# Kernel tuning notes

Measured on AMD Instinct MI355X. Metric: run time of the kernel, lower is better.

The kernel has to match this reference:

```python
import jax, jax.numpy as jnp
import numpy as np

ROI = 116
FEAT = ROI * (ROI - 1) // 2  # 6670 upper-triangular entries
D = 1024
H = 1024
EPS = 1e-5


def _batchnorm(x, gamma, beta):
    # training-mode BatchNorm1d: biased batch statistics over dim 0
    mu = jnp.mean(x, axis=0, keepdims=True)
    var = jnp.var(x, axis=0, keepdims=True)
    return (x - mu) * jax.lax.rsqrt(var + EPS) * gamma + beta


def setup_inputs() -> dict:
    key = jax.random.key(0)
    ks = jax.random.split(key, 16)
    B, W = 64, 128
    s_feat = 1.0 / np.sqrt(FEAT)
    s_d = 1.0 / np.sqrt(D)
    s_cat = 1.0 / np.sqrt(FEAT + H)
    s_h = 1.0 / np.sqrt(H)
    return {
        "FC": jax.random.normal(ks[0], (B, W, ROI, ROI), jnp.float32),
        "cluster_centers": jax.random.normal(ks[1], (2, FEAT), jnp.float32),
        # MIL attention MLP: Linear(6670,1024) -> Tanh -> Linear(1024,1)
        "W1": jax.random.uniform(ks[2], (FEAT, D), jnp.float32, -s_feat, s_feat),
        "b1": jnp.zeros((D,), jnp.float32),
        "W2": jax.random.uniform(ks[3], (D, 1), jnp.float32, -s_d, s_d),
        "b2": jnp.zeros((1,), jnp.float32),
        # batch norms
        "bn_g": jnp.ones((FEAT,), jnp.float32),
        "bn_b": jnp.zeros((FEAT,), jnp.float32),
        "bn2_g": jnp.ones((FEAT,), jnp.float32),
        "bn2_b": jnp.zeros((FEAT,), jnp.float32),
        # cross-attention projections (Wv_cross is dead code in the source)
        "Wq": jax.random.uniform(ks[4], (FEAT, H), jnp.float32, -s_feat, s_feat),
        "bq": jnp.zeros((H,), jnp.float32),
        "Wk": jax.random.uniform(ks[5], (FEAT, H), jnp.float32, -s_feat, s_feat),
        "bk": jnp.zeros((H,), jnp.float32),
        # classifier (dropout = identity at inference)
        "Wc1": jax.random.uniform(ks[6], (FEAT + H, H), jnp.float32, -s_cat, s_cat),
        "bc1": jnp.zeros((H,), jnp.float32),
        "Wc2": jax.random.uniform(ks[7], (H, 1), jnp.float32, -s_h, s_h),
        "bc2": jnp.zeros((1,), jnp.float32),
    }


def reference(FC, cluster_centers, W1, b1, W2, b2, bn_g, bn_b, bn2_g, bn2_b,
              Wq, bq, Wk, bk, Wc1, bc1, Wc2, bc2):
    iu0, iu1 = jnp.triu_indices(ROI, k=1)
    bag_level = FC[:, :, iu0, iu1]                      # [B, W, 6670]

    # MIL attention pooling, batched over samples (replaces per-sample loop)
    h = jnp.tanh(jnp.einsum('bwf,fd->bwd', bag_level, W1) + b1)
    a = jnp.einsum('bwd,dk->bwk', h, W2) + b2           # [B, W, 1]
    att = jax.nn.softmax(a[..., 0], axis=-1)            # softmax over windows
    bag_z_up = jnp.einsum('bw,bwf->bf', att, bag_level)  # [B, 6670]

    bag_z_up = _batchnorm(bag_z_up, bn_g, bn_b)
    cc = _batchnorm(cluster_centers, bn2_g, bn2_b)       # [K, 6670]

    q = bag_z_up @ Wq + bq                               # [B, H]
    k = cc @ Wk + bk                                     # [K, H]
    QK = (q @ k.T) / jnp.sqrt(jnp.float32(H))            # [B, K]
    att_cross = jax.nn.softmax(QK, axis=-1)
    v = cc @ Wq + bq                                     # NB: source reuses Wq_cross
    final_cross = att_cross @ v                          # [B, H]

    X = jnp.concatenate([final_cross, bag_z_up], axis=1)  # [B, H+6670]
    Y_prob = jax.nn.sigmoid(jax.nn.relu(X @ Wc1 + bc1) @ Wc2 + bc2)[:, 0]
    Y_hat = (Y_prob >= 0.5).astype(jnp.float32)
    return Y_prob, Y_hat
```

## Files before the change

kernel.cpp:

```cpp
#include <hip/hip_runtime.h>
#include <hip/hip_bf16.h>
#include <math.h>
#include <stdint.h>

#define ROI   116
#define FEATN 6670
#define KP    6688
#define DD    1024
#define HHN   1024
#define BB    64
#define WW    128
#define MT    8192
#define XW    7694
#define EPSV  1e-5f
#define KB_SPLIT 32

typedef __attribute__((ext_vector_type(8))) short short8;
typedef __attribute__((ext_vector_type(4))) short short4v;
typedef __attribute__((ext_vector_type(4))) float f32x4;
typedef __attribute__((ext_vector_type(4))) unsigned int u32x4;

typedef __attribute__((address_space(3))) unsigned int as3_u32;
typedef __attribute__((address_space(1))) unsigned int as1_u32;

__device__ __forceinline__ void gload_lds16(const void* g, void* l) {
  __builtin_amdgcn_global_load_lds(
      (const as1_u32*)(uintptr_t)g,
      (as3_u32*)(unsigned int)(uintptr_t)l,
      16, 0, 0);
}

__device__ __forceinline__ short f2bf(float v) {
  __hip_bfloat16 b = __float2bfloat16(v);
  return *reinterpret_cast<short*>(&b);
}

__device__ __forceinline__ float bf2f(short h) {
  unsigned int u = ((unsigned int)(unsigned short)h) << 16;
  float f;
  __builtin_memcpy(&f, &u, 4);
  return f;
}

__device__ __forceinline__ float fast_tanh(float x) {
  float ax = fabsf(x);
  float t  = __expf(-2.0f * ax);
  float r  = (1.0f - t) / (1.0f + t);
  return copysignf(r, x);
}

__global__ void k_lut(int2* lut) {
  int f = blockIdx.x * 256 + threadIdx.x;
  if (f >= FEATN) return;
  int i = (int)((231.0 - sqrt((double)(53361 - 8 * f))) * 0.5);
  if (i < 0) i = 0;
  if (i > ROI - 2) i = ROI - 2;
  while (i > 0 && i * (231 - i) / 2 > f) --i;
  while (i < ROI - 2 && (i + 1) * (231 - (i + 1)) / 2 <= f) ++i;
  int j = i + 1 + (f - i * (231 - i) / 2);
  lut[f] = make_int2(i, j);
}

__global__ void k_extract(const float* __restrict__ FC, const int2* __restrict__ lut,
                          short* __restrict__ bag, float* __restrict__ a_out) {
  int m = blockIdx.x;
  if (threadIdx.x == 0) a_out[m] = 0.f;
  const float* base = FC + (size_t)m * (ROI * ROI);
  for (int f0 = threadIdx.x * 4; f0 < KP; f0 += 1024) {
    short4v o;
#pragma unroll
    for (int e = 0; e < 4; e++) {
      int f = f0 + e;
      float v = 0.f;
      if (f < FEATN) {
        int2 ij = lut[f];
        v = base[ij.x * ROI + ij.y];
      }
      o[e] = f2bf(v);
    }
    *(short4v*)(&bag[(size_t)m * KP + f0]) = o;
  }
}

__global__ void k_transpose(const float* __restrict__ W1, short* __restrict__ W1T) {
  __shared__ float tile[32][33];
  int k0 = blockIdx.x * 32;
  int d0 = blockIdx.y * 32;
  int tx = threadIdx.x & 31, ty = threadIdx.x >> 5;
  for (int r = 0; r < 32; r += 8) {
    int k = k0 + ty + r;
    float v = 0.f;
    if (k < FEATN) v = W1[(size_t)k * DD + d0 + tx];
    tile[ty + r][tx] = v;
  }
  __syncthreads();
  for (int r = 0; r < 32; r += 8) {
    W1T[(size_t)(d0 + ty + r) * KP + k0 + tx] = f2bf(tile[tx][ty + r]);
  }
}

__global__ __launch_bounds__(256) void k_gemm(const short* __restrict__ A,
                                              const short* __restrict__ BT,
                                              const float* __restrict__ b1,
                                              const float* __restrict__ W2,
                                              float* __restrict__ a_out) {
  __shared__ __align__(16) short As[128][32];
  __shared__ __align__(16) short Bs[128][32];
  int tid  = threadIdx.x;
  int m0   = blockIdx.x * 128;
  int n0   = blockIdx.y * 128;
  int wave = tid >> 6, lane = tid & 63;
  int wr = wave >> 1, wc = wave & 1;
  int quad = lane >> 4, l15 = lane & 15;
  int srow = tid >> 2;
  int scol = (tid & 3) * 8;

  f32x4 acc[4][4] = {};

  const short* Ag0 = A  + (size_t)(m0 + srow) * KP + scol;
  const short* Ag1 = Ag0 + (size_t)64 * KP;
  const short* Bg0 = BT + (size_t)(n0 + srow) * KP + scol;
  const short* Bg1 = Bg0 + (size_t)64 * KP;
  short* Al0 = &As[srow][scol];
  short* Al1 = &As[srow + 64][scol];
  short* Bl0 = &Bs[srow][scol];
  short* Bl1 = &Bs[srow + 64][scol];

  for (int k0 = 0; k0 < KP; k0 += 32) {
    gload_lds16(Ag0 + k0, Al0);
    gload_lds16(Ag1 + k0, Al1);
    gload_lds16(Bg0 + k0, Bl0);
    gload_lds16(Bg1 + k0, Bl1);
    __syncthreads();

    short8 af[4], bf[4];
#pragma unroll
    for (int mi = 0; mi < 4; mi++)
      af[mi] = *(const short8*)(&As[wr * 64 + mi * 16 + l15][quad * 8]);
#pragma unroll
    for (int ni = 0; ni < 4; ni++)
      bf[ni] = *(const short8*)(&Bs[wc * 64 + ni * 16 + l15][quad * 8]);
#pragma unroll
    for (int mi = 0; mi < 4; mi++)
#pragma unroll
      for (int ni = 0; ni < 4; ni++)
        acc[mi][ni] = __builtin_amdgcn_mfma_f32_16x16x32_bf16(af[mi], bf[ni], acc[mi][ni], 0, 0, 0);
    __syncthreads();
  }

  float bias[4], w2v[4];
#pragma unroll
  for (int ni = 0; ni < 4; ni++) {
    int n = n0 + wc * 64 + ni * 16 + l15;
    bias[ni] = b1[n];
    w2v[ni]  = W2[n];
  }
#pragma unroll
  for (int mi = 0; mi < 4; mi++) {
#pragma unroll
    for (int r = 0; r < 4; r++) {
      float s = 0.f;
#pragma unroll
      for (int ni = 0; ni < 4; ni++)
        s += fast_tanh(acc[mi][ni][r] + bias[ni]) * w2v[ni];
      s += __shfl_xor(s, 1);
      s += __shfl_xor(s, 2);
      s += __shfl_xor(s, 4);
      s += __shfl_xor(s, 8);
      if (l15 == 0)
        atomicAdd(&a_out[m0 + wr * 64 + mi * 16 + quad * 4 + r], s);
    }
  }
}

__global__ void k_softmax(const float* __restrict__ a, float* __restrict__ att) {
  int b = blockIdx.x, t = threadIdx.x;
  __shared__ float sh[128];
  float v = a[b * WW + t];
  sh[t] = v; __syncthreads();
  for (int s = 64; s > 0; s >>= 1) { if (t < s) sh[t] = fmaxf(sh[t], sh[t + s]); __syncthreads(); }
  float mx = sh[0]; __syncthreads();
  float e = expf(v - mx);
  sh[t] = e; __syncthreads();
  for (int s = 64; s > 0; s >>= 1) { if (t < s) sh[t] += sh[t + s]; __syncthreads(); }
  att[b * WW + t] = e / sh[0];
}

__global__ void k_bagz(const short* __restrict__ bag, const float* __restrict__ att,
                       float* __restrict__ bagz) {
  __shared__ float atts[WW];
  int b  = blockIdx.y;
  int f0 = blockIdx.x * 2048 + threadIdx.x * 8;
  if (threadIdx.x < WW) atts[threadIdx.x] = att[b * WW + threadIdx.x];
  __syncthreads();
  if (f0 >= KP) return;
  const short* base = bag + (size_t)b * WW * KP + f0;
  float s[8] = {};
  for (int w = 0; w < WW; ++w) {
    float aw = atts[w];
    short8 v = *(const short8*)(base + (size_t)w * KP);
#pragma unroll
    for (int e = 0; e < 8; e++) s[e] += aw * bf2f(v[e]);
  }
#pragma unroll
  for (int e = 0; e < 8; e++) {
    int f = f0 + e;
    if (f < FEATN) bagz[(size_t)b * FEATN + f] = s[e];
  }
}

__global__ void k_bn(const float* __restrict__ bagz, const float* __restrict__ g,
                     const float* __restrict__ beta, float* __restrict__ X) {
  int f = blockIdx.x * 256 + threadIdx.x;
  if (f >= FEATN) return;
  float s = 0.f, s2 = 0.f;
  for (int b = 0; b < BB; b++) { float v = bagz[(size_t)b * FEATN + f]; s += v; s2 += v * v; }
  float mu  = s * (1.f / BB);
  float var = s2 * (1.f / BB) - mu * mu;
  float sc  = rsqrtf(var + EPSV) * g[f];
  float bt  = beta[f];
  for (int b = 0; b < BB; b++)
    X[(size_t)b * XW + HHN + f] = (bagz[(size_t)b * FEATN + f] - mu) * sc + bt;
}

__global__ void k_ccbn(const float* __restrict__ cc, const float* __restrict__ g,
                       const float* __restrict__ beta, float* __restrict__ ccbn) {
  int f = blockIdx.x * 256 + threadIdx.x;
  if (f >= FEATN) return;
  float c0 = cc[f], c1 = cc[FEATN + f];
  float mu = 0.5f * (c0 + c1);
  float d0 = c0 - mu, d1 = c1 - mu;
  float var = 0.5f * (d0 * d0 + d1 * d1);
  float sc = rsqrtf(var + EPSV) * g[f];
  ccbn[f]         = d0 * sc + beta[f];
  ccbn[FEATN + f] = d1 * sc + beta[f];
}

template <int R, int MODE>
__global__ __launch_bounds__(256) void k_skinny(const float* __restrict__ X,
                                                const float* __restrict__ ccbn,
                                                const float* __restrict__ Wt,
                                                float* __restrict__ partial,
                                                int K, int kchunk) {
  constexpr int RG = (R + 3) / 4;
  constexpr int RP = RG * 4;
  __shared__ __align__(16) float zs[RP][68];
  int tx = threadIdx.x & 63;
  int ty = threadIdx.x >> 6;
  int n  = blockIdx.x * 64 + tx;
  int k0 = blockIdx.y * kchunk;
  int k1 = min(k0 + kchunk, K);
  int r0 = ty * RG;

  float acc[RG];
#pragma unroll
  for (int i = 0; i < RG; i++) acc[i] = 0.f;

  for (int kk0 = k0; kk0 < k1; kk0 += 64) {
    for (int idx = threadIdx.x; idx < RP * 64; idx += 256) {
      int r = idx >> 6, c = idx & 63;
      int k = kk0 + c;
      float v = 0.f;
      if (r < R && k < k1) {
        const float* zr;
        if (MODE == 0) zr = (r < 64) ? (X + (size_t)r * XW + HHN) : (ccbn + (size_t)(r - 64) * FEATN);
        else if (MODE == 1) zr = ccbn + (size_t)r * FEATN;
        else zr = X + (size_t)r * XW;
        v = zr[k];
      }
      zs[r][c] = v;
    }
    __syncthreads();
#pragma unroll 4
    for (int c = 0; c < 64; c += 4) {
      int k = kk0 + c;
      float w0 = (k + 0 < k1) ? Wt[(size_t)(k + 0) * HHN + n] : 0.f;
      float w1 = (k + 1 < k1) ? Wt[(size_t)(k + 1) * HHN + n] : 0.f;
      float w2 = (k + 2 < k1) ? Wt[(size_t)(k + 2) * HHN + n] : 0.f;
      float w3 = (k + 3 < k1) ? Wt[(size_t)(k + 3) * HHN + n] : 0.f;
#pragma unroll
      for (int i = 0; i < RG; i++) {
        f32x4 z = *(const f32x4*)(&zs[r0 + i][c]);
        acc[i] += z.x * w0 + z.y * w1 + z.z * w2 + z.w * w3;
      }
    }
    __syncthreads();
  }
#pragma unroll
  for (int i = 0; i < RG; i++) {
    int rr = r0 + i;
    if (rr < R)
      partial[(size_t)blockIdx.y * R * HHN + (size_t)rr * HHN + n] = acc[i];
  }
}

template <int R>
__global__ void k_reduce(const float* __restrict__ partial, const float* __restrict__ bias,
                         float* __restrict__ out, int KB, int act) {
  int idx = blockIdx.x * 256 + threadIdx.x;
  if (idx >= R * HHN) return;
  int n = idx & (HHN - 1);
  float s = bias[n];
  for (int kb = 0; kb < KB; kb++) s += partial[(size_t)kb * R * HHN + idx];
  if (act) s = fmaxf(s, 0.f);
  out[idx] = s;
}

__global__ void k_cross(const float* __restrict__ qv, const float* __restrict__ kb,
                        float* __restrict__ X) {
  int b = blockIdx.x, t = threadIdx.x;
  const float* q  = qv + (size_t)b * HHN;
  const float* v0 = qv + (size_t)64 * HHN;
  const float* v1 = qv + (size_t)65 * HHN;
  float s0 = 0.f, s1 = 0.f;
  for (int n = t; n < HHN; n += 256) {
    float qn = q[n];
    s0 += qn * kb[n];
    s1 += qn * kb[HHN + n];
  }
  __shared__ float r0[256], r1[256];
  r0[t] = s0; r1[t] = s1; __syncthreads();
  for (int st = 128; st > 0; st >>= 1) {
    if (t < st) { r0[t] += r0[t + st]; r1[t] += r1[t + st]; }
    __syncthreads();
  }
  float d0 = r0[0] * (1.f / 32.f), d1 = r1[0] * (1.f / 32.f);
  float mx = fmaxf(d0, d1);
  float e0 = expf(d0 - mx), e1 = expf(d1 - mx);
  float p0 = e0 / (e0 + e1), p1 = e1 / (e0 + e1);
  for (int n = t; n < HHN; n += 256)
    X[(size_t)b * XW + n] = p0 * v0[n] + p1 * v1[n];
}

__global__ void k_final(const float* __restrict__ Rb, const float* __restrict__ Wc2,
                        const float* __restrict__ bc2, float* __restrict__ out) {
  int b = blockIdx.x, t = threadIdx.x;
  float s = 0.f;
  for (int n = t; n < HHN; n += 256) s += Rb[(size_t)b * HHN + n] * Wc2[n];
  __shared__ float red[256];
  red[t] = s; __syncthreads();
  for (int st = 128; st > 0; st >>= 1) {
    if (t < st) red[t] += red[t + st];
    __syncthreads();
  }
  if (t == 0) {
    float y = red[0] + bc2[0];
    float p = 1.f / (1.f + expf(-y));
    out[b]      = p;
    out[64 + b] = (p >= 0.5f) ? 1.f : 0.f;
  }
}

extern "C" void kernel_launch(void* const* d_in, const int* in_sizes, int n_in,
                              void* d_out, int out_size, void* d_ws, size_t ws_size,
                              hipStream_t stream) {
  const float* FC    = (const float*)d_in[0];
  const float* CC    = (const float*)d_in[1];
  const float* W1    = (const float*)d_in[2];
  const float* b1    = (const float*)d_in[3];
  const float* W2    = (const float*)d_in[4];
  const float* b2    = (const float*)d_in[5];
  const float* bn_g  = (const float*)d_in[6];
  const float* bn_b  = (const float*)d_in[7];
  const float* bn2_g = (const float*)d_in[8];
  const float* bn2_b = (const float*)d_in[9];
  const float* Wq    = (const float*)d_in[10];
  const float* bq    = (const float*)d_in[11];
  const float* Wk    = (const float*)d_in[12];
  const float* bk    = (const float*)d_in[13];
  const float* Wc1   = (const float*)d_in[14];
  const float* bc1   = (const float*)d_in[15];
  const float* Wc2   = (const float*)d_in[16];
  const float* bc2   = (const float*)d_in[17];
  float* out = (float*)d_out;
  (void)b2;

  char* w = (char*)d_ws;
  auto alloc = [&](size_t bytes) {
    char* p = w;
    w += (bytes + 255) & ~(size_t)255;
    return p;
  };
  short* bagbf   = (short*)alloc((size_t)MT * KP * 2);
  short* W1T     = (short*)alloc((size_t)DD * KP * 2);
  float* abuf    = (float*)alloc((size_t)MT * 4);
  float* attbuf  = (float*)alloc((size_t)MT * 4);
  float* bagz    = (float*)alloc((size_t)BB * FEATN * 4);
  float* Xbuf    = (float*)alloc((size_t)BB * XW * 4);
  float* ccbn    = (float*)alloc((size_t)2 * FEATN * 4);
  float* qvbuf   = (float*)alloc((size_t)66 * HHN * 4);
  float* kbuf    = (float*)alloc((size_t)2 * HHN * 4);
  float* Rbuf    = (float*)alloc((size_t)BB * HHN * 4);
  int2*  lut     = (int2*)alloc((size_t)FEATN * 8);
  float* partQ   = (float*)alloc((size_t)KB_SPLIT * 66 * HHN * 4);
  float* partK   = (float*)alloc((size_t)KB_SPLIT * 2 * HHN * 4);
  float* partC   = partQ;

  k_lut<<<dim3((FEATN + 255) / 256), dim3(256), 0, stream>>>(lut);
  k_extract<<<dim3(MT), dim3(256), 0, stream>>>(FC, lut, bagbf, abuf);
  k_transpose<<<dim3(KP / 32, DD / 32), dim3(256), 0, stream>>>(W1, W1T);
  k_gemm<<<dim3(MT / 128, DD / 128), dim3(256), 0, stream>>>(bagbf, W1T, b1, W2, abuf);
  k_softmax<<<dim3(BB), dim3(WW), 0, stream>>>(abuf, attbuf);
  k_bagz<<<dim3((KP + 2047) / 2048, BB), dim3(256), 0, stream>>>(bagbf, attbuf, bagz);
  k_bn<<<dim3((FEATN + 255) / 256), dim3(256), 0, stream>>>(bagz, bn_g, bn_b, Xbuf);
  k_ccbn<<<dim3((FEATN + 255) / 256), dim3(256), 0, stream>>>(CC, bn2_g, bn2_b, ccbn);

  k_skinny<66, 0><<<dim3(16, KB_SPLIT), dim3(256), 0, stream>>>(Xbuf, ccbn, Wq, partQ, FEATN, 209);
  k_reduce<66><<<dim3(66 * HHN / 256), dim3(256), 0, stream>>>(partQ, bq, qvbuf, KB_SPLIT, 0);
  k_skinny<2, 1><<<dim3(16, KB_SPLIT), dim3(256), 0, stream>>>(Xbuf, ccbn, Wk, partK, FEATN, 209);
  k_reduce<2><<<dim3(2 * HHN / 256), dim3(256), 0, stream>>>(partK, bk, kbuf, KB_SPLIT, 0);
  k_cross<<<dim3(BB), dim3(256), 0, stream>>>(qvbuf, kbuf, Xbuf);

  k_skinny<64, 2><<<dim3(16, KB_SPLIT), dim3(256), 0, stream>>>(Xbuf, ccbn, Wc1, partC, XW, 241);
  k_reduce<64><<<dim3(64 * HHN / 256), dim3(256), 0, stream>>>(partC, bc1, Rbuf, KB_SPLIT, 1);
  k_final<<<dim3(BB), dim3(256), 0, stream>>>(Rbuf, Wc2, bc2, out);

  (void)in_sizes; (void)n_in; (void)out_size; (void)ws_size;
}
```

Baseline: 1.166 ms.

## Fuse small pipeline kernels and split bag pooling across window slices

Merges the LUT, extract and W1 transpose into one prep kernel that computes triangular indices inline. Softmax is folded into the bag pooling kernel, which now splits the windows into four slices and writes partial sums. The batchnorm kernel adds those partials and also normalises the cluster centers, and the Q and K skinny GEMMs and their reductions run as single launches. The aim is fewer launches and more parallelism in the bagz stage, at the cost of extra partial-sum traffic and per-block redundant softmax work.

```diff
diff --git a/kernel.cpp b/kernel.cpp
--- a/kernel.cpp
+++ b/kernel.cpp
@@ -14,9 +14,10 @@
 #define XW    7694
 #define EPSV  1e-5f
 #define KB_SPLIT 32
+#define NTB   6688
+#define WS    4
 
 typedef __attribute__((ext_vector_type(8))) short short8;
-typedef __attribute__((ext_vector_type(4))) short short4v;
 typedef __attribute__((ext_vector_type(4))) float f32x4;
 typedef __attribute__((ext_vector_type(4))) unsigned int u32x4;
 
@@ -49,53 +50,48 @@
   return copysignf(r, x);
 }
 
-__global__ void k_lut(int2* lut) {
-  int f = blockIdx.x * 256 + threadIdx.x;
-  if (f >= FEATN) return;
-  int i = (int)((231.0 - sqrt((double)(53361 - 8 * f))) * 0.5);
-  if (i < 0) i = 0;
-  if (i > ROI - 2) i = ROI - 2;
-  while (i > 0 && i * (231 - i) / 2 > f) --i;
-  while (i < ROI - 2 && (i + 1) * (231 - (i + 1)) / 2 <= f) ++i;
-  int j = i + 1 + (f - i * (231 - i) / 2);
-  lut[f] = make_int2(i, j);
-}
-
-__global__ void k_extract(const float* __restrict__ FC, const int2* __restrict__ lut,
-                          short* __restrict__ bag, float* __restrict__ a_out) {
-  int m = blockIdx.x;
-  if (threadIdx.x == 0) a_out[m] = 0.f;
-  const float* base = FC + (size_t)m * (ROI * ROI);
-  for (int f0 = threadIdx.x * 4; f0 < KP; f0 += 1024) {
-    short4v o;
-#pragma unroll
-    for (int e = 0; e < 4; e++) {
-      int f = f0 + e;
+__global__ __launch_bounds__(256) void k_prep(const float* __restrict__ FC,
+                                              const float* __restrict__ W1,
+                                              short* __restrict__ bag,
+                                              short* __restrict__ W1T,
+                                              float* __restrict__ a_out) {
+  __shared__ float tile[32][33];
+  int bx = blockIdx.x;
+  if (bx < MT) {
+    int m = bx;
+    if (threadIdx.x == 0) a_out[m] = 0.f;
+    const float* base = FC + (size_t)m * (ROI * ROI);
+    for (int f0 = threadIdx.x * 8; f0 < KP; f0 += 2048) {
+      int fc = min(f0, FEATN - 1);
+      int i = (int)((231.0f - sqrtf((float)(53361 - 8 * fc))) * 0.5f);
+      i = max(0, min(i, ROI - 2));
+      while (i > 0 && i * (231 - i) / 2 > fc) --i;
+      while (i < ROI - 2 && (i + 1) * (231 - (i + 1)) / 2 <= fc) ++i;
+      int j = i + 1 + (fc - i * (231 - i) / 2);
+      short8 o;
+#pragma unroll
+      for (int e = 0; e < 8; e++) {
+        float v = 0.f;
+        if (f0 + e < FEATN) v = base[i * ROI + j];
+        o[e] = f2bf(v);
+        if (++j == ROI) { ++i; j = i + 1; }
+      }
+      *(short8*)(&bag[(size_t)m * KP + f0]) = o;
+    }
+  } else {
+    int t2 = bx - MT;
+    int k0 = (t2 % (KP / 32)) * 32;
+    int d0 = (t2 / (KP / 32)) * 32;
+    int tx = threadIdx.x & 31, ty = threadIdx.x >> 5;
+    for (int r = 0; r < 32; r += 8) {
+      int k = k0 + ty + r;
       float v = 0.f;
-      if (f < FEATN) {
-        int2 ij = lut[f];
-        v = base[ij.x * ROI + ij.y];
-      }
-      o[e] = f2bf(v);
-    }
-    *(short4v*)(&bag[(size_t)m * KP + f0]) = o;
-  }
-}
-
-__global__ void k_transpose(const float* __restrict__ W1, short* __restrict__ W1T) {
-  __shared__ float tile[32][33];
-  int k0 = blockIdx.x * 32;
-  int d0 = blockIdx.y * 32;
-  int tx = threadIdx.x & 31, ty = threadIdx.x >> 5;
-  for (int r = 0; r < 32; r += 8) {
-    int k = k0 + ty + r;
-    float v = 0.f;
-    if (k < FEATN) v = W1[(size_t)k * DD + d0 + tx];
-    tile[ty + r][tx] = v;
-  }
-  __syncthreads();
-  for (int r = 0; r < 32; r += 8) {
-    W1T[(size_t)(d0 + ty + r) * KP + k0 + tx] = f2bf(tile[tx][ty + r]);
+      if (k < FEATN) v = W1[(size_t)k * DD + d0 + tx];
+      tile[ty + r][tx] = v;
+    }
+    __syncthreads();
+    for (int r = 0; r < 32; r += 8)
+      W1T[(size_t)(d0 + ty + r) * KP + k0 + tx] = f2bf(tile[tx][ty + r]);
   }
 }
 
@@ -133,18 +129,18 @@
     gload_lds16(Bg1 + k0, Bl1);
     __syncthreads();
 
-    short8 af[4], bf[4];
+    short8 af[4], bfm[4];
 #pragma unroll
     for (int mi = 0; mi < 4; mi++)
       af[mi] = *(const short8*)(&As[wr * 64 + mi * 16 + l15][quad * 8]);
 #pragma unroll
     for (int ni = 0; ni < 4; ni++)
-      bf[ni] = *(const short8*)(&Bs[wc * 64 + ni * 16 + l15][quad * 8]);
+      bfm[ni] = *(const short8*)(&Bs[wc * 64 + ni * 16 + l15][quad * 8]);
 #pragma unroll
     for (int mi = 0; mi < 4; mi++)
 #pragma unroll
       for (int ni = 0; ni < 4; ni++)
-        acc[mi][ni] = __builtin_amdgcn_mfma_f32_16x16x32_bf16(af[mi], bf[ni], acc[mi][ni], 0, 0, 0);
+        acc[mi][ni] = __builtin_amdgcn_mfma_f32_16x16x32_bf16(af[mi], bfm[ni], acc[mi][ni], 0, 0, 0);
     __syncthreads();
   }
 
@@ -173,75 +169,92 @@
   }
 }
 
-__global__ void k_softmax(const float* __restrict__ a, float* __restrict__ att) {
-  int b = blockIdx.x, t = threadIdx.x;
-  __shared__ float sh[128];
-  float v = a[b * WW + t];
-  sh[t] = v; __syncthreads();
-  for (int s = 64; s > 0; s >>= 1) { if (t < s) sh[t] = fmaxf(sh[t], sh[t + s]); __syncthreads(); }
-  float mx = sh[0]; __syncthreads();
-  float e = expf(v - mx);
-  sh[t] = e; __syncthreads();
-  for (int s = 64; s > 0; s >>= 1) { if (t < s) sh[t] += sh[t + s]; __syncthreads(); }
-  att[b * WW + t] = e / sh[0];
-}
-
-__global__ void k_bagz(const short* __restrict__ bag, const float* __restrict__ att,
-                       float* __restrict__ bagz) {
-  __shared__ float atts[WW];
-  int b  = blockIdx.y;
-  int f0 = blockIdx.x * 2048 + threadIdx.x * 8;
-  if (threadIdx.x < WW) atts[threadIdx.x] = att[b * WW + threadIdx.x];
+__global__ __launch_bounds__(256) void k_bagz(const short* __restrict__ bag,
+                                              const float* __restrict__ abuf,
+                                              float* __restrict__ bagzp) {
+  __shared__ float sm[WW];
+  __shared__ float red[64];
+  int b = blockIdx.y, ws = blockIdx.z, t = threadIdx.x;
+  if (t < WW) sm[t] = abuf[b * WW + t];
   __syncthreads();
+  if (t < 64) red[t] = fmaxf(sm[t], sm[t + 64]);
+  __syncthreads();
+  for (int s = 32; s > 0; s >>= 1) { if (t < s) red[t] = fmaxf(red[t], red[t + s]); __syncthreads(); }
+  float mx = red[0];
+  __syncthreads();
+  if (t < WW) sm[t] = expf(sm[t] - mx);
+  __syncthreads();
+  if (t < 64) red[t] = sm[t] + sm[t + 64];
+  __syncthreads();
+  for (int s = 32; s > 0; s >>= 1) { if (t < s) red[t] += red[t + s]; __syncthreads(); }
+  float inv = 1.f / red[0];
+
+  int f0 = blockIdx.x * 2048 + t * 8;
   if (f0 >= KP) return;
-  const short* base = bag + (size_t)b * WW * KP + f0;
+  const short* base = bag + ((size_t)b * WW + ws * (WW / WS)) * KP + f0;
   float s[8] = {};
-  for (int w = 0; w < WW; ++w) {
-    float aw = atts[w];
+  for (int w = 0; w < WW / WS; ++w) {
+    float aw = sm[ws * (WW / WS) + w] * inv;
     short8 v = *(const short8*)(base + (size_t)w * KP);
 #pragma unroll
     for (int e = 0; e < 8; e++) s[e] += aw * bf2f(v[e]);
   }
+  float* dst = bagzp + ((size_t)ws * BB + b) * FEATN;
 #pragma unroll
   for (int e = 0; e < 8; e++) {
     int f = f0 + e;
-    if (f < FEATN) bagz[(size_t)b * FEATN + f] = s[e];
-  }
-}
-
-__global__ void k_bn(const float* __restrict__ bagz, const float* __restrict__ g,
-                     const float* __restrict__ beta, float* __restrict__ X) {
-  int f = blockIdx.x * 256 + threadIdx.x;
-  if (f >= FEATN) return;
-  float s = 0.f, s2 = 0.f;
-  for (int b = 0; b < BB; b++) { float v = bagz[(size_t)b * FEATN + f]; s += v; s2 += v * v; }
-  float mu  = s * (1.f / BB);
-  float var = s2 * (1.f / BB) - mu * mu;
-  float sc  = rsqrtf(var + EPSV) * g[f];
-  float bt  = beta[f];
-  for (int b = 0; b < BB; b++)
-    X[(size_t)b * XW + HHN + f] = (bagz[(size_t)b * FEATN + f] - mu) * sc + bt;
-}
-
-__global__ void k_ccbn(const float* __restrict__ cc, const float* __restrict__ g,
-                       const float* __restrict__ beta, float* __restrict__ ccbn) {
-  int f = blockIdx.x * 256 + threadIdx.x;
-  if (f >= FEATN) return;
-  float c0 = cc[f], c1 = cc[FEATN + f];
-  float mu = 0.5f * (c0 + c1);
-  float d0 = c0 - mu, d1 = c1 - mu;
-  float var = 0.5f * (d0 * d0 + d1 * d1);
-  float sc = rsqrtf(var + EPSV) * g[f];
-  ccbn[f]         = d0 * sc + beta[f];
-  ccbn[FEATN + f] = d1 * sc + beta[f];
+    if (f < FEATN) dst[f] = s[e];
+  }
+}
+
+__global__ void k_bnall(const float* __restrict__ bagzp, const float* __restrict__ g,
+                        const float* __restrict__ beta, const float* __restrict__ cc,
+                        const float* __restrict__ g2, const float* __restrict__ b2v,
+                        float* __restrict__ X, float* __restrict__ ccbn) {
+  int t = threadIdx.x;
+  if (blockIdx.x < 27) {
+    int f = blockIdx.x * 256 + t;
+    if (f >= FEATN) return;
+    float s = 0.f, s2 = 0.f;
+#pragma unroll
+    for (int b = 0; b < BB; b++) {
+      float x = bagzp[(size_t)b * FEATN + f]
+              + bagzp[((size_t)BB + b) * FEATN + f]
+              + bagzp[((size_t)2 * BB + b) * FEATN + f]
+              + bagzp[((size_t)3 * BB + b) * FEATN + f];
+      s += x; s2 += x * x;
+    }
+    float mu  = s * (1.f / BB);
+    float var = s2 * (1.f / BB) - mu * mu;
+    float sc  = rsqrtf(var + EPSV) * g[f];
+    float bt  = beta[f];
+#pragma unroll
+    for (int b = 0; b < BB; b++) {
+      float x = bagzp[(size_t)b * FEATN + f]
+              + bagzp[((size_t)BB + b) * FEATN + f]
+              + bagzp[((size_t)2 * BB + b) * FEATN + f]
+              + bagzp[((size_t)3 * BB + b) * FEATN + f];
+      X[(size_t)b * XW + HHN + f] = (x - mu) * sc + bt;
+    }
+  } else {
+    int f = (blockIdx.x - 27) * 256 + t;
+    if (f >= FEATN) return;
+    float c0 = cc[f], c1 = cc[FEATN + f];
+    float mu = 0.5f * (c0 + c1);
+    float d0 = c0 - mu, d1 = c1 - mu;
+    float var = 0.5f * (d0 * d0 + d1 * d1);
+    float sc = rsqrtf(var + EPSV) * g2[f];
+    ccbn[f]         = d0 * sc + b2v[f];
+    ccbn[FEATN + f] = d1 * sc + b2v[f];
+  }
 }
 
 template <int R, int MODE>
-__global__ __launch_bounds__(256) void k_skinny(const float* __restrict__ X,
-                                                const float* __restrict__ ccbn,
-                                                const float* __restrict__ Wt,
-                                                float* __restrict__ partial,
-                                                int K, int kchunk) {
+__device__ __forceinline__ void skinny_body(const float* __restrict__ X,
+                                            const float* __restrict__ ccbn,
+                                            const float* __restrict__ Wt,
+                                            float* __restrict__ partial,
+                                            int K, int kchunk) {
   constexpr int RG = (R + 3) / 4;
   constexpr int RP = RG * 4;
   __shared__ __align__(16) float zs[RP][68];
@@ -291,6 +304,40 @@
     int rr = r0 + i;
     if (rr < R)
       partial[(size_t)blockIdx.y * R * HHN + (size_t)rr * HHN + n] = acc[i];
+  }
+}
+
+__global__ __launch_bounds__(256) void k_qk(const float* __restrict__ X,
+                                            const float* __restrict__ ccbn,
+                                            const float* __restrict__ Wq,
+                                            const float* __restrict__ Wk,
+                                            float* __restrict__ partQ,
+                                            float* __restrict__ partK) {
+  if (blockIdx.z == 0) skinny_body<66, 0>(X, ccbn, Wq, partQ, FEATN, 209);
+  else                 skinny_body<2, 1>(X, ccbn, Wk, partK, FEATN, 209);
+}
+
+__global__ __launch_bounds__(256) void k_skinnyC(const float* __restrict__ X,
+                                                 const float* __restrict__ Wt,
+                                                 float* __restrict__ partial) {
+  skinny_body<64, 2>(X, nullptr, Wt, partial, XW, 241);
+}
+
+__global__ void k_redqk(const float* __restrict__ partQ, const float* __restrict__ partK,
+                        const float* __restrict__ bq, const float* __restrict__ bk,
+                        float* __restrict__ qv, float* __restrict__ kb) {
+  int idx = blockIdx.x * 256 + threadIdx.x;
+  if (idx < 66 * HHN) {
+    int n = idx & (HHN - 1);
+    float s = bq[n];
+    for (int kbk = 0; kbk < KB_SPLIT; kbk++) s += partQ[(size_t)kbk * 66 * HHN + idx];
+    qv[idx] = s;
+  } else {
+    int id2 = idx - 66 * HHN;
+    int n = id2 & (HHN - 1);
+    float s = bk[n];
+    for (int kbk = 0; kbk < KB_SPLIT; kbk++) s += partK[(size_t)kbk * 2 * HHN + id2];
+    kb[id2] = s;
   }
 }
 
@@ -384,34 +431,26 @@
   short* bagbf   = (short*)alloc((size_t)MT * KP * 2);
   short* W1T     = (short*)alloc((size_t)DD * KP * 2);
   float* abuf    = (float*)alloc((size_t)MT * 4);
-  float* attbuf  = (float*)alloc((size_t)MT * 4);
-  float* bagz    = (float*)alloc((size_t)BB * FEATN * 4);
+  float* bagzp   = (float*)alloc((size_t)WS * BB * FEATN * 4);
   float* Xbuf    = (float*)alloc((size_t)BB * XW * 4);
   float* ccbn    = (float*)alloc((size_t)2 * FEATN * 4);
   float* qvbuf   = (float*)alloc((size_t)66 * HHN * 4);
   float* kbuf    = (float*)alloc((size_t)2 * HHN * 4);
   float* Rbuf    = (float*)alloc((size_t)BB * HHN * 4);
-  int2*  lut     = (int2*)alloc((size_t)FEATN * 8);
   float* partQ   = (float*)alloc((size_t)KB_SPLIT * 66 * HHN * 4);
   float* partK   = (float*)alloc((size_t)KB_SPLIT * 2 * HHN * 4);
   float* partC   = partQ;
 
-  k_lut<<<dim3((FEATN + 255) / 256), dim3(256), 0, stream>>>(lut);
-  k_extract<<<dim3(MT), dim3(256), 0, stream>>>(FC, lut, bagbf, abuf);
-  k_transpose<<<dim3(KP / 32, DD / 32), dim3(256), 0, stream>>>(W1, W1T);
+  k_prep<<<dim3(MT + NTB), dim3(256), 0, stream>>>(FC, W1, bagbf, W1T, abuf);
   k_gemm<<<dim3(MT / 128, DD / 128), dim3(256), 0, stream>>>(bagbf, W1T, b1, W2, abuf);
-  k_softmax<<<dim3(BB), dim3(WW), 0, stream>>>(abuf, attbuf);
-  k_bagz<<<dim3((KP + 2047) / 2048, BB), dim3(256), 0, stream>>>(bagbf, attbuf, bagz);
-  k_bn<<<dim3((FEATN + 255) / 256), dim3(256), 0, stream>>>(bagz, bn_g, bn_b, Xbuf);
-  k_ccbn<<<dim3((FEATN + 255) / 256), dim3(256), 0, stream>>>(CC, bn2_g, bn2_b, ccbn);
-
-  k_skinny<66, 0><<<dim3(16, KB_SPLIT), dim3(256), 0, stream>>>(Xbuf, ccbn, Wq, partQ, FEATN, 209);
-  k_reduce<66><<<dim3(66 * HHN / 256), dim3(256), 0, stream>>>(partQ, bq, qvbuf, KB_SPLIT, 0);
-  k_skinny<2, 1><<<dim3(16, KB_SPLIT), dim3(256), 0, stream>>>(Xbuf, ccbn, Wk, partK, FEATN, 209);
-  k_reduce<2><<<dim3(2 * HHN / 256), dim3(256), 0, stream>>>(partK, bk, kbuf, KB_SPLIT, 0);
+  k_bagz<<<dim3(4, BB, WS), dim3(256), 0, stream>>>(bagbf, abuf, bagzp);
+  k_bnall<<<dim3(54), dim3(256), 0, stream>>>(bagzp, bn_g, bn_b, CC, bn2_g, bn2_b, Xbuf, ccbn);
+
+  k_qk<<<dim3(16, KB_SPLIT, 2), dim3(256), 0, stream>>>(Xbuf, ccbn, Wq, Wk, partQ, partK);
+  k_redqk<<<dim3(68 * HHN / 256), dim3(256), 0, stream>>>(partQ, partK, bq, bk, qvbuf, kbuf);
   k_cross<<<dim3(BB), dim3(256), 0, stream>>>(qvbuf, kbuf, Xbuf);
 
-  k_skinny<64, 2><<<dim3(16, KB_SPLIT), dim3(256), 0, stream>>>(Xbuf, ccbn, Wc1, partC, XW, 241);
+  k_skinnyC<<<dim3(16, KB_SPLIT), dim3(256), 0, stream>>>(Xbuf, Wc1, partC);
   k_reduce<64><<<dim3(64 * HHN / 256), dim3(256), 0, stream>>>(partC, bc1, Rbuf, KB_SPLIT, 1);
   k_final<<<dim3(BB), dim3(256), 0, stream>>>(Rbuf, Wc2, bc2, out);
 
```

After: 1.249 ms. 7.2% more time.
